# Kernel optimization log

Measured on AMD Instinct MI355X. Metric: run time of the kernel, lower is better.

The kernel has to match this reference:

```python
import jax, jax.numpy as jnp
import numpy as np

N = 8192      # number of samples (x.shape[0])
D = 64        # out_feat / spectral embedding dim
K_NN = 32     # config['school']['k']
KP1 = 64      # columns in idx (>= K_NN + 1)
N_PROJ_ITERS = 100  # Newton iterations for simplex projection


def setup_inputs() -> dict:
    key = jax.random.key(0)
    k1, k2, k3, k4 = jax.random.split(key, 4)
    Y = jax.random.normal(k1, (N, D), jnp.float32)
    semantic_H = jax.random.normal(k2, (N, D), jnp.float32)
    ortho_H = jax.random.normal(k3, (N, D), jnp.float32)
    idx = jax.random.randint(k4, (N, KP1), 0, N)
    return {"Y": Y, "semantic_H": semantic_H, "ortho_H": ortho_H,
            "idx": idx, "alpha": 1, "beta": 1}


def eproj_simplex_rows(v, k=1.0):
    """Project each row of v onto the simplex {x >= 0, sum(x) = k}.
    Fixed-iteration Newton solve for the Lagrange multiplier (matches the
    iterative EProjSimplex_new_matrix; it is a fixed point once converged)."""
    n = v.shape[1]
    v0 = v - v.mean(axis=1, keepdims=True) + k / n   # shift so sum(v0) = k per row

    def body(_, lam):
        v1 = v0 - lam[:, None]
        pos = v1 > 0
        npos = jnp.maximum(pos.sum(axis=1), 1)       # -g
        f = jnp.where(pos, v1, 0.0).sum(axis=1) - k  # constraint residual
        return lam + f / npos                         # lam - f/g

    lam = jax.lax.fori_loop(0, N_PROJ_ITERS, body,
                            jnp.zeros(v.shape[0], v.dtype))
    return jnp.maximum(v0 - lam[:, None], 0.0)


def reference(Y, semantic_H, ortho_H, idx, alpha, beta):
    num = Y.shape[0]
    idxa0 = idx[:, 1:K_NN + 1]                                   # [N, k]
    # kNN gather + pairwise L2 distances (O(N*k*d), no dense NxN distances)
    dfi = jnp.sqrt(((Y[:, None, :] - Y[idxa0]) ** 2).sum(-1) + 1e-8)          # [N, k]
    dxi = jnp.sqrt(((ortho_H[:, None, :] - ortho_H[idxa0]) ** 2).sum(-1) + 1e-8)
    ad = -(dxi + beta * dfi) / (2 * alpha)
    w = eproj_simplex_rows(ad)                                   # [N, k] simplex weights
    # scatter into dense NxN adjacency (faithful to A.scatter_(1, idxa0, w))
    rows = jnp.arange(num)[:, None]
    A = jnp.zeros((num, num), Y.dtype).at[rows, idxa0].set(w)
    embs_hom = A @ semantic_H                                    # [N, D]
    return embs_hom, A, Y
```

## Files before the change

### kernel.cpp

```cpp
#include <hip/hip_runtime.h>

#define NROWS 8192
#define DDIM  64
#define KNN   32
#define MAXIT 100

__device__ __forceinline__ float scalar_val(const void* p) {
    int iv = *(const int*)p;
    if (iv > -1000000 && iv < 1000000) return (float)iv;
    return *(const float*)p;
}

__global__ __launch_bounds__(256, 6) void school_fused_kernel(
    const float* __restrict__ Y,
    const float* __restrict__ semH,
    const float* __restrict__ orthoH,
    const int*   __restrict__ idx,
    const void*  alpha_p,
    const void*  beta_p,
    float* __restrict__ embs,
    float* __restrict__ A,
    float* __restrict__ Yout)
{
    __shared__ int    col_s[8][KNN];
    __shared__ float  ad_s[8][KNN];
    __shared__ float2 cw_s[8][KNN];

    const int tid  = threadIdx.x;
    const int j    = tid & 31;
    const int r    = tid >> 5;
    const int row0 = blockIdx.x * 8;
    const int row  = row0 + r;

    const float alpha = scalar_val(alpha_p);
    const float beta  = scalar_val(beta_p);

    const int col = idx[row * 64 + 1 + j];
    col_s[r][j] = col;

    const float4* Y4 = (const float4*)Y;
    const float4* O4 = (const float4*)orthoH;
    const int q = j & 15;
    const float4 ownY = Y4[(size_t)row * 16 + q];
    const float4 ownO = O4[(size_t)row * 16 + q];

    #pragma unroll 2
    for (int t = 0; t < 16; ++t) {
        const int c = col_s[r][2 * t + (j >> 4)];
        const float4 gY = Y4[(size_t)c * 16 + q];
        const float4 gO = O4[(size_t)c * 16 + q];
        float ex = ownY.x - gY.x, ey = ownY.y - gY.y,
              ez = ownY.z - gY.z, ew = ownY.w - gY.w;
        float dY = ex * ex + ey * ey + ez * ez + ew * ew;
        ex = ownO.x - gO.x; ey = ownO.y - gO.y;
        ez = ownO.z - gO.z; ew = ownO.w - gO.w;
        float dO = ex * ex + ey * ey + ez * ez + ew * ew;
        #pragma unroll
        for (int mm = 1; mm <= 8; mm <<= 1) {
            dY += __shfl_xor(dY, mm, 64);
            dO += __shfl_xor(dO, mm, 64);
        }
        if ((j & 15) == 0) {
            float dfv = sqrtf(dY + 1e-8f);
            float dxv = sqrtf(dO + 1e-8f);
            ad_s[r][2 * t + (j >> 4)] = -(dxv + beta * dfv) / (2.f * alpha);
        }
    }
    const float ad = ad_s[r][j];

    float s = ad;
    #pragma unroll
    for (int mm = 1; mm <= 16; mm <<= 1) s += __shfl_xor(s, mm, 64);
    const float v0 = ad - s * (1.f / 32.f) + (1.f / 32.f);

    float lam = 0.f;
    #pragma unroll 1
    for (int it = 0; it < MAXIT; ++it) {
        float v1 = v0 - lam;
        float p = v1 > 0.f ? v1 : 0.f;
        float c = v1 > 0.f ? 1.f : 0.f;
        #pragma unroll
        for (int mm = 1; mm <= 16; mm <<= 1) {
            p += __shfl_xor(p, mm, 64);
            c += __shfl_xor(c, mm, 64);
        }
        float step = (p - 1.f) / fmaxf(c, 1.f);
        lam += step;
        if (__all(fabsf(step) <= 1e-6f ? 1 : 0)) break;
    }
    const float w = fmaxf(v0 - lam, 0.f);

    bool dead = false;
    for (int jj = j + 1; jj < 32; ++jj)
        dead |= (col_s[r][jj] == col);
    cw_s[r][j] = make_float2(__int_as_float(col), dead ? 0.f : w);

    {
        float2 acc = make_float2(0.f, 0.f);
        const float2* H2 = (const float2*)semH;
        #pragma unroll 4
        for (int jj = 0; jj < KNN; ++jj) {
            float2 cw = cw_s[r][jj];
            int   c   = __float_as_int(cw.x);
            float wv  = cw.y;
            float2 h = H2[(size_t)c * 32 + j];
            acc.x += wv * h.x;
            acc.y += wv * h.y;
        }
        ((float2*)embs)[(size_t)row * 32 + j] = acc;
    }

    {
        const float2* Y2 = (const float2*)(Y + (size_t)row0 * DDIM);
        float2* O2 = (float2*)(Yout + (size_t)row0 * DDIM);
        O2[tid] = Y2[tid];
    }

    unsigned k0 = 0xFFFFFFFFu, k1 = 0xFFFFFFFFu, k2 = 0xFFFFFFFFu, k3 = 0xFFFFFFFFu;
    float f0 = 0.f, f1 = 0.f, f2 = 0.f, f3 = 0.f;
    int nhit = 0;
    #pragma unroll 1
    for (int jj = 0; jj < 32; ++jj) {
        float2 cw = cw_s[r][jj];
        int c = __float_as_int(cw.x);
        if (((c >> 2) & 31) == j) {
            unsigned key = ((unsigned)(c >> 7) << 2) | (unsigned)(c & 3);
            float wv = cw.y;
            k3 = (nhit == 3) ? key : k3;  f3 = (nhit == 3) ? wv : f3;
            k2 = (nhit == 2) ? key : k2;  f2 = (nhit == 2) ? wv : f2;
            k1 = (nhit == 1) ? key : k1;  f1 = (nhit == 1) ? wv : f1;
            k0 = (nhit == 0) ? key : k0;  f0 = (nhit == 0) ? wv : f0;
            nhit++;
        }
    }

    {
        float4* Arow4 = (float4*)(A + (size_t)row * NROWS);
        #pragma unroll 4
        for (int ss = 0; ss < 64; ++ss) {
            float4 v = make_float4(0.f, 0.f, 0.f, 0.f);
            #define APPLY_SLOT(kk, ff)                                   \
                if ((kk >> 2) == (unsigned)ss) {                         \
                    int p_ = (int)(kk & 3u);                             \
                    v.x = (p_ == 0) ? ff : v.x;                          \
                    v.y = (p_ == 1) ? ff : v.y;                          \
                    v.z = (p_ == 2) ? ff : v.z;                          \
                    v.w = (p_ == 3) ? ff : v.w;                          \
                }
            APPLY_SLOT(k0, f0)
            APPLY_SLOT(k1, f1)
            APPLY_SLOT(k2, f2)
            APPLY_SLOT(k3, f3)
            #undef APPLY_SLOT
            Arow4[(ss << 5) + j] = v;
        }
    }

    if (nhit > 4) {
        asm volatile("s_waitcnt vmcnt(0)" ::: "memory");
        int cnt = 0;
        for (int jj = 0; jj < 32; ++jj) {
            float2 cw = cw_s[r][jj];
            int c = __float_as_int(cw.x);
            if (((c >> 2) & 31) == j) {
                if (cnt >= 4) {
                    A[(size_t)row * NROWS + c] = cw.y;
                    asm volatile("s_waitcnt vmcnt(0)" ::: "memory");
                }
                cnt++;
            }
        }
    }
}

extern "C" void kernel_launch(void* const* d_in, const int* in_sizes, int n_in,
                              void* d_out, int out_size, void* d_ws, size_t ws_size,
                              hipStream_t stream) {
    const float* Y      = (const float*)d_in[0];
    const float* semH   = (const float*)d_in[1];
    const float* orthoH = (const float*)d_in[2];
    const int*   idx    = (const int*)d_in[3];
    const void*  alpha  = d_in[4];
    const void*  beta   = d_in[5];

    float* out  = (float*)d_out;
    float* embs = out;
    float* A    = out + (size_t)NROWS * DDIM;
    float* Yout = A + (size_t)NROWS * NROWS;

    school_fused_kernel<<<NROWS / 8, 256, 0, stream>>>(
        Y, semH, orthoH, idx, alpha, beta, embs, A, Yout);
}
```

Baseline: 63.37 us.

## Split block into zero-fill waves and compute waves for dense adjacency writes

Warp specialization: two of the four wavefronts now only write zeros to the dense A rows, skipping the float4 slots that hold neighbour weights. The other two wavefronts each handle two rows for distances, simplex projection and the embedding gather, then write only the slots that hold nonzero weights. The aim is to overlap the bandwidth-bound zero-fill of the 256MB adjacency with the latency-bound Newton iterations. In exchange, compute parallelism per block is halved, and the launch-bounds occupancy hint drops from 6 to 4.

Result: slower. 85.67 us (+35.2%).

```diff
diff --git a/kernel.cpp b/kernel.cpp
--- a/kernel.cpp
+++ b/kernel.cpp
@@ -11,7 +11,7 @@
     return *(const float*)p;
 }
 
-__global__ __launch_bounds__(256, 6) void school_fused_kernel(
+__global__ __launch_bounds__(256, 4) void school_fused_kernel(
     const float* __restrict__ Y,
     const float* __restrict__ semH,
     const float* __restrict__ orthoH,
@@ -25,149 +25,209 @@
     __shared__ int    col_s[8][KNN];
     __shared__ float  ad_s[8][KNN];
     __shared__ float2 cw_s[8][KNN];
+    __shared__ int    zcol[2][2][64];
 
     const int tid  = threadIdx.x;
-    const int j    = tid & 31;
-    const int r    = tid >> 5;
+    const int wv   = tid >> 6;
     const int row0 = blockIdx.x * 8;
-    const int row  = row0 + r;
+
+    if (wv >= 2) {
+        const int wz = wv - 2;
+        const int L  = tid & 63;
+        const int h  = L >> 5;
+        const int j  = L & 31;
+        const int ra0 = wz * 4 + h;
+        const int ra1 = wz * 4 + 2 + h;
+
+        const int c0 = idx[(row0 + ra0) * 64 + 1 + j];
+        const int c1 = idx[(row0 + ra1) * 64 + 1 + j];
+        zcol[wz][0][L] = c0;
+        zcol[wz][1][L] = c1;
+
+        unsigned long long m0 = 0ull, m1 = 0ull;
+        #pragma unroll 1
+        for (int jj = 0; jj < 32; ++jj) {
+            int a = zcol[wz][0][h * 32 + jj];
+            int b = zcol[wz][1][h * 32 + jj];
+            if (((a >> 2) & 31) == j) m0 |= 1ull << (a >> 7);
+            if (((b >> 2) & 31) == j) m1 |= 1ull << (b >> 7);
+        }
+
+        const float4 z4 = make_float4(0.f, 0.f, 0.f, 0.f);
+        float4* R0 = (float4*)(A + (size_t)(row0 + ra0) * NROWS);
+        float4* R1 = (float4*)(A + (size_t)(row0 + ra1) * NROWS);
+        #pragma unroll 8
+        for (int ss = 0; ss < 64; ++ss)
+            if (!((m0 >> ss) & 1ull)) R0[(ss << 5) + j] = z4;
+        #pragma unroll 8
+        for (int ss = 0; ss < 64; ++ss)
+            if (!((m1 >> ss) & 1ull)) R1[(ss << 5) + j] = z4;
+        return;
+    }
+
+    const int hw = tid >> 5;
+    const int j  = tid & 31;
 
     const float alpha = scalar_val(alpha_p);
     const float beta  = scalar_val(beta_p);
 
-    const int col = idx[row * 64 + 1 + j];
-    col_s[r][j] = col;
-
     const float4* Y4 = (const float4*)Y;
     const float4* O4 = (const float4*)orthoH;
-    const int q = j & 15;
-    const float4 ownY = Y4[(size_t)row * 16 + q];
-    const float4 ownO = O4[(size_t)row * 16 + q];
-
-    #pragma unroll 2
-    for (int t = 0; t < 16; ++t) {
-        const int c = col_s[r][2 * t + (j >> 4)];
-        const float4 gY = Y4[(size_t)c * 16 + q];
-        const float4 gO = O4[(size_t)c * 16 + q];
-        float ex = ownY.x - gY.x, ey = ownY.y - gY.y,
-              ez = ownY.z - gY.z, ew = ownY.w - gY.w;
-        float dY = ex * ex + ey * ey + ez * ez + ew * ew;
-        ex = ownO.x - gO.x; ey = ownO.y - gO.y;
-        ez = ownO.z - gO.z; ew = ownO.w - gO.w;
-        float dO = ex * ex + ey * ey + ez * ez + ew * ew;
+
+    #pragma unroll 1
+    for (int rr = 0; rr < 2; ++rr) {
+        const int row_rel = hw * 2 + rr;
+        const int row     = row0 + row_rel;
+
+        const int col = idx[row * 64 + 1 + j];
+        col_s[row_rel][j] = col;
+
+        const int q = j & 15, g = j >> 4;
+        const float4 ownY = Y4[(size_t)row * 16 + q];
+        const float4 ownO = O4[(size_t)row * 16 + q];
+
+        #pragma unroll 4
+        for (int t = 0; t < 16; ++t) {
+            const int c = col_s[row_rel][2 * t + g];
+            const float4 gY = Y4[(size_t)c * 16 + q];
+            const float4 gO = O4[(size_t)c * 16 + q];
+            float ex = ownY.x - gY.x, ey = ownY.y - gY.y,
+                  ez = ownY.z - gY.z, ew = ownY.w - gY.w;
+            float dY = ex * ex + ey * ey + ez * ez + ew * ew;
+            ex = ownO.x - gO.x; ey = ownO.y - gO.y;
+            ez = ownO.z - gO.z; ew = ownO.w - gO.w;
+            float dO = ex * ex + ey * ey + ez * ez + ew * ew;
+            #pragma unroll
+            for (int mm = 1; mm <= 8; mm <<= 1) {
+                dY += __shfl_xor(dY, mm, 64);
+                dO += __shfl_xor(dO, mm, 64);
+            }
+            if ((j & 15) == 0) {
+                float dfv = sqrtf(dY + 1e-8f);
+                float dxv = sqrtf(dO + 1e-8f);
+                ad_s[row_rel][2 * t + g] = -(dxv + beta * dfv) / (2.f * alpha);
+            }
+        }
+        const float ad = ad_s[row_rel][j];
+
+        float s = ad;
         #pragma unroll
-        for (int mm = 1; mm <= 8; mm <<= 1) {
-            dY += __shfl_xor(dY, mm, 64);
-            dO += __shfl_xor(dO, mm, 64);
-        }
-        if ((j & 15) == 0) {
-            float dfv = sqrtf(dY + 1e-8f);
-            float dxv = sqrtf(dO + 1e-8f);
-            ad_s[r][2 * t + (j >> 4)] = -(dxv + beta * dfv) / (2.f * alpha);
-        }
-    }
-    const float ad = ad_s[r][j];
-
-    float s = ad;
-    #pragma unroll
-    for (int mm = 1; mm <= 16; mm <<= 1) s += __shfl_xor(s, mm, 64);
-    const float v0 = ad - s * (1.f / 32.f) + (1.f / 32.f);
-
-    float lam = 0.f;
-    #pragma unroll 1
-    for (int it = 0; it < MAXIT; ++it) {
-        float v1 = v0 - lam;
-        float p = v1 > 0.f ? v1 : 0.f;
-        float c = v1 > 0.f ? 1.f : 0.f;
-        #pragma unroll
-        for (int mm = 1; mm <= 16; mm <<= 1) {
-            p += __shfl_xor(p, mm, 64);
-            c += __shfl_xor(c, mm, 64);
-        }
-        float step = (p - 1.f) / fmaxf(c, 1.f);
-        lam += step;
-        if (__all(fabsf(step) <= 1e-6f ? 1 : 0)) break;
-    }
-    const float w = fmaxf(v0 - lam, 0.f);
-
-    bool dead = false;
-    for (int jj = j + 1; jj < 32; ++jj)
-        dead |= (col_s[r][jj] == col);
-    cw_s[r][j] = make_float2(__int_as_float(col), dead ? 0.f : w);
+        for (int mm = 1; mm <= 16; mm <<= 1) s += __shfl_xor(s, mm, 64);
+        const float v0 = ad - s * (1.f / 32.f) + (1.f / 32.f);
+
+        float lam = 0.f;
+        #pragma unroll 1
+        for (int it = 0; it < MAXIT; ++it) {
+            float v1 = v0 - lam;
+            float p = v1 > 0.f ? v1 : 0.f;
+            float c = v1 > 0.f ? 1.f : 0.f;
+            #pragma unroll
+            for (int mm = 1; mm <= 16; mm <<= 1) {
+                p += __shfl_xor(p, mm, 64);
+                c += __shfl_xor(c, mm, 64);
+            }
+            float step = (p - 1.f) / fmaxf(c, 1.f);
+            lam += step;
+            if (__all(fabsf(step) <= 1e-6f ? 1 : 0)) break;
+        }
+        const float w = fmaxf(v0 - lam, 0.f);
+
+        bool dead = false;
+        for (int jj = j + 1; jj < 32; ++jj)
+            dead |= (col_s[row_rel][jj] == col);
+        cw_s[row_rel][j] = make_float2(__int_as_float(col), dead ? 0.f : w);
+    }
 
     {
-        float2 acc = make_float2(0.f, 0.f);
         const float2* H2 = (const float2*)semH;
-        #pragma unroll 4
-        for (int jj = 0; jj < KNN; ++jj) {
-            float2 cw = cw_s[r][jj];
-            int   c   = __float_as_int(cw.x);
-            float wv  = cw.y;
-            float2 h = H2[(size_t)c * 32 + j];
-            acc.x += wv * h.x;
-            acc.y += wv * h.y;
-        }
-        ((float2*)embs)[(size_t)row * 32 + j] = acc;
+        #pragma unroll 1
+        for (int rr = 0; rr < 2; ++rr) {
+            const int row_rel = hw * 2 + rr;
+            const int row     = row0 + row_rel;
+            float2 acc = make_float2(0.f, 0.f);
+            #pragma unroll 4
+            for (int jj = 0; jj < KNN; ++jj) {
+                float2 cw = cw_s[row_rel][jj];
+                int   c   = __float_as_int(cw.x);
+                float wv  = cw.y;
+                float2 hl = H2[(size_t)c * 32 + j];
+                acc.x += wv * hl.x;
+                acc.y += wv * hl.y;
+            }
+            ((float2*)embs)[(size_t)row * 32 + j] = acc;
+        }
     }
 
     {
         const float2* Y2 = (const float2*)(Y + (size_t)row0 * DDIM);
         float2* O2 = (float2*)(Yout + (size_t)row0 * DDIM);
-        O2[tid] = Y2[tid];
-    }
-
-    unsigned k0 = 0xFFFFFFFFu, k1 = 0xFFFFFFFFu, k2 = 0xFFFFFFFFu, k3 = 0xFFFFFFFFu;
-    float f0 = 0.f, f1 = 0.f, f2 = 0.f, f3 = 0.f;
-    int nhit = 0;
+        O2[tid]       = Y2[tid];
+        O2[tid + 128] = Y2[tid + 128];
+    }
+
     #pragma unroll 1
-    for (int jj = 0; jj < 32; ++jj) {
-        float2 cw = cw_s[r][jj];
-        int c = __float_as_int(cw.x);
-        if (((c >> 2) & 31) == j) {
-            unsigned key = ((unsigned)(c >> 7) << 2) | (unsigned)(c & 3);
-            float wv = cw.y;
-            k3 = (nhit == 3) ? key : k3;  f3 = (nhit == 3) ? wv : f3;
-            k2 = (nhit == 2) ? key : k2;  f2 = (nhit == 2) ? wv : f2;
-            k1 = (nhit == 1) ? key : k1;  f1 = (nhit == 1) ? wv : f1;
-            k0 = (nhit == 0) ? key : k0;  f0 = (nhit == 0) ? wv : f0;
-            nhit++;
-        }
-    }
-
-    {
-        float4* Arow4 = (float4*)(A + (size_t)row * NROWS);
-        #pragma unroll 4
-        for (int ss = 0; ss < 64; ++ss) {
-            float4 v = make_float4(0.f, 0.f, 0.f, 0.f);
-            #define APPLY_SLOT(kk, ff)                                   \
-                if ((kk >> 2) == (unsigned)ss) {                         \
-                    int p_ = (int)(kk & 3u);                             \
-                    v.x = (p_ == 0) ? ff : v.x;                          \
-                    v.y = (p_ == 1) ? ff : v.y;                          \
-                    v.z = (p_ == 2) ? ff : v.z;                          \
-                    v.w = (p_ == 3) ? ff : v.w;                          \
-                }
-            APPLY_SLOT(k0, f0)
-            APPLY_SLOT(k1, f1)
-            APPLY_SLOT(k2, f2)
-            APPLY_SLOT(k3, f3)
-            #undef APPLY_SLOT
-            Arow4[(ss << 5) + j] = v;
-        }
-    }
-
-    if (nhit > 4) {
-        asm volatile("s_waitcnt vmcnt(0)" ::: "memory");
-        int cnt = 0;
+    for (int rr = 0; rr < 2; ++rr) {
+        const int row_rel = hw * 2 + rr;
+        const int row     = row0 + row_rel;
+
+        unsigned long long hm = 0ull;
+        unsigned k0 = 0xFFFFFFFFu, k1 = 0xFFFFFFFFu,
+                 k2 = 0xFFFFFFFFu, k3 = 0xFFFFFFFFu;
+        float f0 = 0.f, f1 = 0.f, f2 = 0.f, f3 = 0.f;
+        int nhit = 0;
+        #pragma unroll 1
         for (int jj = 0; jj < 32; ++jj) {
-            float2 cw = cw_s[r][jj];
+            float2 cw = cw_s[row_rel][jj];
             int c = __float_as_int(cw.x);
             if (((c >> 2) & 31) == j) {
-                if (cnt >= 4) {
-                    A[(size_t)row * NROWS + c] = cw.y;
-                    asm volatile("s_waitcnt vmcnt(0)" ::: "memory");
+                hm |= 1ull << (c >> 7);
+                unsigned key = ((unsigned)(c >> 7) << 2) | (unsigned)(c & 3);
+                float wvv = cw.y;
+                k3 = (nhit == 3) ? key : k3;  f3 = (nhit == 3) ? wvv : f3;
+                k2 = (nhit == 2) ? key : k2;  f2 = (nhit == 2) ? wvv : f2;
+                k1 = (nhit == 1) ? key : k1;  f1 = (nhit == 1) ? wvv : f1;
+                k0 = (nhit == 0) ? key : k0;  f0 = (nhit == 0) ? wvv : f0;
+                nhit++;
+            }
+        }
+
+        {
+            float4* Arow4 = (float4*)(A + (size_t)row * NROWS);
+            unsigned long long mrem = hm;
+            while (mrem) {
+                int ss = __ffsll(mrem) - 1;
+                mrem &= mrem - 1;
+                float4 v = make_float4(0.f, 0.f, 0.f, 0.f);
+                #define APPLY_SLOT(kk, ff)                                   \
+                    if ((int)(kk >> 2) == ss) {                              \
+                        int p_ = (int)(kk & 3u);                             \
+                        v.x = (p_ == 0) ? ff : v.x;                          \
+                        v.y = (p_ == 1) ? ff : v.y;                          \
+                        v.z = (p_ == 2) ? ff : v.z;                          \
+                        v.w = (p_ == 3) ? ff : v.w;                          \
+                    }
+                APPLY_SLOT(k0, f0)
+                APPLY_SLOT(k1, f1)
+                APPLY_SLOT(k2, f2)
+                APPLY_SLOT(k3, f3)
+                #undef APPLY_SLOT
+                Arow4[(ss << 5) + j] = v;
+            }
+        }
+
+        if (nhit > 4) {
+            asm volatile("s_waitcnt vmcnt(0)" ::: "memory");
+            int cnt = 0;
+            for (int jj = 0; jj < 32; ++jj) {
+                float2 cw = cw_s[row_rel][jj];
+                int c = __float_as_int(cw.x);
+                if (((c >> 2) & 31) == j) {
+                    if (cnt >= 4) {
+                        A[(size_t)row * NROWS + c] = cw.y;
+                        asm volatile("s_waitcnt vmcnt(0)" ::: "memory");
+                    }
+                    cnt++;
                 }
-                cnt++;
             }
         }
     }
```

## Split fused kernel into compute and dense-adjacency expansion kernels

Applied to the files above, without the earlier changes.

Splits the single fused kernel into two. The first computes distances, simplex weights, embeddings and the Y copy, and writes (column, weight) pairs to workspace. The second reads those pairs and streams the dense NxN adjacency rows. The aim is a register-light, pure-streaming write kernel for the dominant A store. Launch bounds also drop from 6 to 4 waves, and the gather loop unroll is raised. The cost is an extra launch, a workspace round-trip, and no overlap of compute with the A writes.

New measurement: 68.63 us. 1.08x slower.

```diff
diff --git a/kernel.cpp b/kernel.cpp
--- a/kernel.cpp
+++ b/kernel.cpp
@@ -11,7 +11,7 @@
     return *(const float*)p;
 }
 
-__global__ __launch_bounds__(256, 6) void school_fused_kernel(
+__global__ __launch_bounds__(256, 4) void school_compute_kernel(
     const float* __restrict__ Y,
     const float* __restrict__ semH,
     const float* __restrict__ orthoH,
@@ -19,7 +19,7 @@
     const void*  alpha_p,
     const void*  beta_p,
     float* __restrict__ embs,
-    float* __restrict__ A,
+    float2* __restrict__ ws,
     float* __restrict__ Yout)
 {
     __shared__ int    col_s[8][KNN];
@@ -40,13 +40,13 @@
 
     const float4* Y4 = (const float4*)Y;
     const float4* O4 = (const float4*)orthoH;
-    const int q = j & 15;
+    const int q = j & 15, g = j >> 4;
     const float4 ownY = Y4[(size_t)row * 16 + q];
     const float4 ownO = O4[(size_t)row * 16 + q];
 
-    #pragma unroll 2
+    #pragma unroll 4
     for (int t = 0; t < 16; ++t) {
-        const int c = col_s[r][2 * t + (j >> 4)];
+        const int c = col_s[r][2 * t + g];
         const float4 gY = Y4[(size_t)c * 16 + q];
         const float4 gO = O4[(size_t)c * 16 + q];
         float ex = ownY.x - gY.x, ey = ownY.y - gY.y,
@@ -63,7 +63,7 @@
         if ((j & 15) == 0) {
             float dfv = sqrtf(dY + 1e-8f);
             float dxv = sqrtf(dO + 1e-8f);
-            ad_s[r][2 * t + (j >> 4)] = -(dxv + beta * dfv) / (2.f * alpha);
+            ad_s[r][2 * t + g] = -(dxv + beta * dfv) / (2.f * alpha);
         }
     }
     const float ad = ad_s[r][j];
@@ -93,16 +93,18 @@
     bool dead = false;
     for (int jj = j + 1; jj < 32; ++jj)
         dead |= (col_s[r][jj] == col);
-    cw_s[r][j] = make_float2(__int_as_float(col), dead ? 0.f : w);
+    const float2 cw = make_float2(__int_as_float(col), dead ? 0.f : w);
+    cw_s[r][j] = cw;
+    ws[(size_t)row * KNN + j] = cw;
 
     {
         float2 acc = make_float2(0.f, 0.f);
         const float2* H2 = (const float2*)semH;
         #pragma unroll 4
         for (int jj = 0; jj < KNN; ++jj) {
-            float2 cw = cw_s[r][jj];
-            int   c   = __float_as_int(cw.x);
-            float wv  = cw.y;
+            float2 c2 = cw_s[r][jj];
+            int   c   = __float_as_int(c2.x);
+            float wv  = c2.y;
             float2 h = H2[(size_t)c * 32 + j];
             acc.x += wv * h.x;
             acc.y += wv * h.y;
@@ -115,6 +117,21 @@
         float2* O2 = (float2*)(Yout + (size_t)row0 * DDIM);
         O2[tid] = Y2[tid];
     }
+}
+
+__global__ __launch_bounds__(256, 4) void school_expand_kernel(
+    const float2* __restrict__ ws,
+    float* __restrict__ A)
+{
+    __shared__ float2 cw_s[8][KNN];
+
+    const int tid  = threadIdx.x;
+    const int j    = tid & 31;
+    const int r    = tid >> 5;
+    const int row  = blockIdx.x * 8 + r;
+
+    const float2 mycw = ws[(size_t)row * KNN + j];
+    cw_s[r][j] = mycw;
 
     unsigned k0 = 0xFFFFFFFFu, k1 = 0xFFFFFFFFu, k2 = 0xFFFFFFFFu, k3 = 0xFFFFFFFFu;
     float f0 = 0.f, f1 = 0.f, f2 = 0.f, f3 = 0.f;
@@ -188,6 +205,10 @@
     float* A    = out + (size_t)NROWS * DDIM;
     float* Yout = A + (size_t)NROWS * NROWS;
 
-    school_fused_kernel<<<NROWS / 8, 256, 0, stream>>>(
-        Y, semH, orthoH, idx, alpha, beta, embs, A, Yout);
-}
+    float2* ws = (float2*)d_ws;
+
+    school_compute_kernel<<<NROWS / 8, 256, 0, stream>>>(
+        Y, semH, orthoH, idx, alpha, beta, embs, ws, Yout);
+
+    school_expand_kernel<<<NROWS / 8, 256, 0, stream>>>(ws, A);
+}
```
